# Kernel optimization log

Measured on AMD Instinct MI355X. Metric: run time of the kernel, lower is better.

The kernel has to match this reference:

```python
import jax, jax.numpy as jnp
import numpy as np

B, N, I, K = 2, 8192, 3, 10
LEN_IN = 3 * (K + 1) + 3 * K + I  # 69


def setup_inputs() -> dict:
    key = jax.random.key(0)
    ks = jax.random.split(key, 9)
    return {
        "position": jax.random.normal(ks[0], (B, N, 3), dtype=jnp.float32),
        "velocity": jax.random.normal(ks[1], (B, N, 3), dtype=jnp.float32),
        "init_config": jax.random.normal(ks[2], (B, I), dtype=jnp.float32),
        "W1": jax.random.normal(ks[3], (LEN_IN, 32), dtype=jnp.float32) * 0.1,
        "b1": jnp.zeros((32,), dtype=jnp.float32),
        "W2": jax.random.normal(ks[4], (32, 16), dtype=jnp.float32) * 0.1,
        "b2": jnp.zeros((16,), dtype=jnp.float32),
        "W3": jax.random.normal(ks[5], (16, 6), dtype=jnp.float32) * 0.1,
        "b3": jnp.zeros((6,), dtype=jnp.float32),
    }


def reference(position, velocity, init_config, W1, b1, W2, b2, W3, b3):
    b, n, _ = position.shape
    k = K
    # Squared Euclidean distances (same k-NN ordering as torch.cdist).
    sq = jnp.sum(position * position, axis=-1)  # [B,N]
    d2 = sq[:, :, None] + sq[:, None, :] - 2.0 * jnp.einsum(
        "bnd,bmd->bnm", position, position
    )  # [B,N,N]
    # k+1 nearest (self included), sorted ascending by distance.
    _, idx = jax.lax.top_k(-d2, k + 1)  # [B,N,k+1]
    # Gather neighbor velocities (incl. self) and positions (excl. self).
    vel_nn = jnp.take_along_axis(
        velocity[:, None, :, :], idx[..., None], axis=2
    )  # [B,N,k+1,3]
    pos_nn = jnp.take_along_axis(
        position[:, None, :, :], idx[:, :, 1:, None], axis=2
    )  # [B,N,k,3]
    offset = pos_nn - position[:, :, None, :]  # [B,N,k,3]
    feats = jnp.concatenate(
        [
            vel_nn.reshape(b, n, 3 * (k + 1)),
            offset.reshape(b, n, 3 * k),
            jnp.broadcast_to(init_config[:, None, :], (b, n, init_config.shape[-1])),
        ],
        axis=-1,
    )  # [B,N,6k+3+I]
    h = feats @ W1 + b1
    h = h @ W2 + b2
    pred = h @ W3 + b3  # [B,N,6]
    pred = jnp.concatenate([pred[..., :3] + position, pred[..., 3:]], axis=-1)
    return pred
```

## Files before the change

### kernel.cpp

```cpp
#include <hip/hip_runtime.h>

#define NPTS   8192
#define KNN    11
#define QPB    64
#define NTHR   1024
#define NSLICE 16
#define SLEN   (NPTS / NSLICE)
#define DEPTH  10
#define TRIG   7

__global__ __launch_bounds__(NTHR, 4) void knn_mlp(
    const float* __restrict__ pos,
    const float* __restrict__ vel,
    const float* __restrict__ initc,
    const float* __restrict__ W1,
    const float* __restrict__ b1,
    const float* __restrict__ W2,
    const float* __restrict__ b2,
    const float* __restrict__ W3,
    const float* __restrict__ b3,
    float* __restrict__ out) {

    __shared__ __align__(16) char smem[32 * 1024 + NTHR * DEPTH * 8];
    __shared__ float sW[405];

    float* ssq = (float*)smem;
    unsigned long long* region = (unsigned long long*)(smem + 32 * 1024);

    const int tid  = threadIdx.x;
    const int lane = tid & 63;
    const int wave = tid >> 6;
    const int b    = blockIdx.x >> 7;
    const int n0   = (blockIdx.x & 127) * QPB;
    const int q    = n0 + lane;

    const float* posb = pos + b * NPTS * 3;
    const float* velb = vel + b * NPTS * 3;

    for (int a = tid; a < NPTS; a += NTHR) {
        float x = posb[a * 3 + 0];
        float y = posb[a * 3 + 1];
        float z = posb[a * 3 + 2];
        ssq[a] = __fmaf_rn(z, z, __fmaf_rn(y, y, __fmul_rn(x, x)));
    }
    float* sW12 = (float*)region;
    for (int e = tid; e < 66 * 16; e += NTHR) {
        int r = e >> 4, c = e & 15;
        float s = 0.f;
        for (int j = 0; j < 32; ++j) s += W1[r * 32 + j] * W2[j * 16 + c];
        sW12[e] = s;
    }
    if (tid < 16) {
        float s = b2[tid];
        for (int j = 0; j < 32; ++j) s += b1[j] * W2[j * 16 + tid];
        sW12[66 * 16 + tid] = s;
    }
    if (tid < 3) sW[402 + tid] = initc[b * 3 + tid];
    __syncthreads();
    for (int e = tid; e < 66 * 6; e += NTHR) {
        int r = e / 6, c = e - r * 6;
        float s = 0.f;
        for (int j = 0; j < 16; ++j) s += sW12[r * 16 + j] * W3[j * 6 + c];
        sW[e] = s;
    }
    if (tid < 6) {
        float s = b3[tid];
        for (int j = 0; j < 16; ++j) s += sW12[66 * 16 + j] * W3[j * 6 + tid];
        sW[396 + tid] = s;
    }
    __syncthreads();

    const float qx = posb[q * 3 + 0];
    const float qy = posb[q * 3 + 1];
    const float qz = posb[q * 3 + 2];
    const float sqq = ssq[q];

    float d0 = 3.0e38f, d1 = 3.0e38f, d2v = 3.0e38f, d3 = 3.0e38f, d4 = 3.0e38f,
          d5 = 3.0e38f, d6 = 3.0e38f, d7 = 3.0e38f, d8 = 3.0e38f, d9 = 3.0e38f,
          d10 = 3.0e38f;
    int   i0 = 0x7FFFFFFF, i1 = 0x7FFFFFFF, i2v = 0x7FFFFFFF, i3 = 0x7FFFFFFF,
          i4 = 0x7FFFFFFF, i5 = 0x7FFFFFFF, i6 = 0x7FFFFFFF, i7 = 0x7FFFFFFF,
          i8 = 0x7FFFFFFF, i9 = 0x7FFFFFFF, i10 = 0x7FFFFFFF;

    float thr = 3.0e38f;
    int cnt = 0;

    auto insert = [&](float nd, int nj) {
        if (nd < d10) {
            bool c, cp;
            cp = nd < d9;  d10 = cp ? d9  : nd;             i10 = cp ? i9  : nj;             c = cp;
            cp = nd < d8;  d9  = cp ? d8  : (c ? nd : d9);  i9  = cp ? i8  : (c ? nj : i9);  c = cp;
            cp = nd < d7;  d8  = cp ? d7  : (c ? nd : d8);  i8  = cp ? i7  : (c ? nj : i8);  c = cp;
            cp = nd < d6;  d7  = cp ? d6  : (c ? nd : d7);  i7  = cp ? i6  : (c ? nj : i7);  c = cp;
            cp = nd < d5;  d6  = cp ? d5  : (c ? nd : d6);  i6  = cp ? i5  : (c ? nj : i6);  c = cp;
            cp = nd < d4;  d5  = cp ? d4  : (c ? nd : d5);  i5  = cp ? i4  : (c ? nj : i5);  c = cp;
            cp = nd < d3;  d4  = cp ? d3  : (c ? nd : d4);  i4  = cp ? i3  : (c ? nj : i4);  c = cp;
            cp = nd < d2v; d3  = cp ? d2v : (c ? nd : d3);  i3  = cp ? i2v : (c ? nj : i3);  c = cp;
            cp = nd < d1;  d2v = cp ? d1  : (c ? nd : d2v); i2v = cp ? i1  : (c ? nj : i2v); c = cp;
            cp = nd < d0;  d1  = cp ? d0  : (c ? nd : d1);  i1  = cp ? i0  : (c ? nj : i1);  c = cp;
            if (c) { d0 = nd; i0 = nj; }
        }
    };

    auto flush = [&]() {
#pragma unroll 1
        for (int k = 0; __any(k < cnt); ++k) {
            if (k < cnt) {
                unsigned long long e = region[k * NTHR + tid];
                float nd = __uint_as_float((unsigned)(e >> 32));
                int   nj = (int)(unsigned)(e & 0xFFFFFFFFull);
                insert(nd, nj);
            }
        }
        cnt = 0;
        thr = d10;
    };

    auto proc = [&](float cx, float cy, float cz, float sqc, int j) {
        float dot = __fmaf_rn(qz, cz, __fmaf_rn(qy, cy, __fmul_rn(qx, cx)));
        float dd  = __fmaf_rn(-2.0f, dot, __fadd_rn(sqq, sqc));
        if (dd < thr) {
            region[cnt * NTHR + tid] =
                (((unsigned long long)__float_as_uint(dd)) << 32) | (unsigned)j;
            ++cnt;
        }
    };

    const int base = wave * SLEN;
    const float4* gp = (const float4*)(posb + base * 3);
    const float4* sp = (const float4*)(ssq + base);
#pragma unroll 1
    for (int m = 0; m < SLEN; m += 4) {
        int f = (m >> 2) * 3;
        float4 A = gp[f], Bv = gp[f + 1], C = gp[f + 2];
        float4 S = sp[m >> 2];
        int j = base + m;
        proc(A.x,  A.y,  A.z,  S.x, j + 0);
        proc(A.w,  Bv.x, Bv.y, S.y, j + 1);
        proc(Bv.z, Bv.w, C.x,  S.z, j + 2);
        proc(C.y,  C.z,  C.w,  S.w, j + 3);
        if (__any(cnt >= TRIG)) flush();
    }
    flush();

    __syncthreads();
    float* pd = (float*)smem;
    int*   pi = (int*)(smem + NTHR * KNN * 4);
    {
        float* pw = pd + tid * KNN;
        int*   iw = pi + tid * KNN;
        pw[0] = d0;  pw[1] = d1;  pw[2] = d2v; pw[3] = d3;  pw[4] = d4;
        pw[5] = d5;  pw[6] = d6;  pw[7] = d7;  pw[8] = d8;  pw[9] = d9;
        pw[10] = d10;
        iw[0] = i0;  iw[1] = i1;  iw[2] = i2v; iw[3] = i3;  iw[4] = i4;
        iw[5] = i5;  iw[6] = i6;  iw[7] = i7;  iw[8] = i8;  iw[9] = i9;
        iw[10] = i10;
    }
    __syncthreads();

    if (tid < QPB) {
        int p[NSLICE]; float hd[NSLICE]; int hi[NSLICE];
#pragma unroll
        for (int s = 0; s < NSLICE; ++s) {
            p[s]  = 0;
            hd[s] = pd[(s * 64 + tid) * KNN];
            hi[s] = pi[(s * 64 + tid) * KNN];
        }
        float acc[6];
#pragma unroll
        for (int c = 0; c < 6; ++c) acc[c] = sW[396 + c];

        for (int r = 0; r < KNN; ++r) {
            float bd = 3.9e38f; int bi = 0x7FFFFFFF; int bs = 0;
#pragma unroll
            for (int s = 0; s < NSLICE; ++s) {
                bool better = (hd[s] < bd) || (hd[s] == bd && hi[s] < bi);
                bs = better ? s : bs;
                bi = better ? hi[s] : bi;
                bd = better ? hd[s] : bd;
            }
            {
                int pp = ++p[bs];
                if (pp < KNN) {
                    hd[bs] = pd[(bs * 64 + tid) * KNN + pp];
                    hi[bs] = pi[(bs * 64 + tid) * KNN + pp];
                } else { hd[bs] = 3.9e38f; hi[bs] = 0x7FFFFFFF; }
            }

            int bg = ((unsigned)bi < (unsigned)NPTS) ? bi : 0;

            const float* vp = velb + bg * 3;
            float vx = vp[0], vy = vp[1], vz = vp[2];
            const float* w = &sW[r * 18];
#pragma unroll
            for (int c = 0; c < 6; ++c) {
                acc[c] += vx * w[c];
                acc[c] += vy * w[6 + c];
                acc[c] += vz * w[12 + c];
            }
            if (r >= 1) {
                float ox = posb[bg * 3 + 0] - qx;
                float oy = posb[bg * 3 + 1] - qy;
                float oz = posb[bg * 3 + 2] - qz;
                const float* w2 = &sW[(33 + (r - 1) * 3) * 6];
#pragma unroll
                for (int c = 0; c < 6; ++c) {
                    acc[c] += ox * w2[c];
                    acc[c] += oy * w2[6 + c];
                    acc[c] += oz * w2[12 + c];
                }
            }
        }
#pragma unroll
        for (int k3 = 0; k3 < 3; ++k3) {
            const float* w3 = &sW[(63 + k3) * 6];
            float iv = sW[402 + k3];
#pragma unroll
            for (int c = 0; c < 6; ++c) acc[c] += iv * w3[c];
        }
        acc[0] += qx; acc[1] += qy; acc[2] += qz;

        float* op = out + (b * NPTS + q) * 6;
#pragma unroll
        for (int c = 0; c < 6; ++c) op[c] = acc[c];
    }
}

extern "C" void kernel_launch(void* const* d_in, const int* in_sizes, int n_in,
                              void* d_out, int out_size, void* d_ws, size_t ws_size,
                              hipStream_t stream) {
    (void)in_sizes; (void)n_in; (void)out_size; (void)d_ws; (void)ws_size;
    const float* pos   = (const float*)d_in[0];
    const float* vel   = (const float*)d_in[1];
    const float* initc = (const float*)d_in[2];
    const float* W1    = (const float*)d_in[3];
    const float* b1    = (const float*)d_in[4];
    const float* W2    = (const float*)d_in[5];
    const float* b2    = (const float*)d_in[6];
    const float* W3    = (const float*)d_in[7];
    const float* b3    = (const float*)d_in[8];
    float* out = (float*)d_out;

    knn_mlp<<<256, NTHR, 0, stream>>>(pos, vel, initc, W1, b1, W2, b2, W3, b3, out);
}
```

Baseline: 175.3 us.

## Share per-query kNN thresholds across slice waves at two rendezvous points

Each of the 16 waves scans its own slice of candidates with a private top-11 threshold. The scan is now split into three phases, with two block-wide rendezvous points in between. At each point the waves publish their current 11th-best distance to shared memory, take the minimum across slices, and nudge it up by one ulp so that exact ties are still admitted. That tighter global bound reduces candidate pushes and flushes in later phases, at the cost of two extra __syncthreads and a small shared array.

```diff
diff --git a/kernel.cpp b/kernel.cpp
--- a/kernel.cpp
+++ b/kernel.cpp
@@ -8,6 +8,8 @@
 #define SLEN   (NPTS / NSLICE)
 #define DEPTH  10
 #define TRIG   7
+#define REND1  32
+#define REND2  128
 
 __global__ __launch_bounds__(NTHR, 4) void knn_mlp(
     const float* __restrict__ pos,
@@ -23,6 +25,7 @@
 
     __shared__ __align__(16) char smem[32 * 1024 + NTHR * DEPTH * 8];
     __shared__ float sW[405];
+    __shared__ float thrS[NSLICE][QPB];
 
     float* ssq = (float*)smem;
     unsigned long long* region = (unsigned long long*)(smem + 32 * 1024);
@@ -82,7 +85,8 @@
           i4 = 0x7FFFFFFF, i5 = 0x7FFFFFFF, i6 = 0x7FFFFFFF, i7 = 0x7FFFFFFF,
           i8 = 0x7FFFFFFF, i9 = 0x7FFFFFFF, i10 = 0x7FFFFFFF;
 
-    float thr = 3.0e38f;
+    float thrR = 3.0e38f;
+    float thr  = 3.0e38f;
     int cnt = 0;
 
     auto insert = [&](float nd, int nj) {
@@ -113,7 +117,24 @@
             }
         }
         cnt = 0;
-        thr = d10;
+        thr = fminf(d10, thrR);
+    };
+
+    auto rendezvous = [&]() {
+        flush();
+        thrS[wave][lane] = d10;
+        __syncthreads();
+        float bm = thrS[0][lane];
+#pragma unroll
+        for (int w = 1; w < NSLICE; ++w) bm = fminf(bm, thrS[w][lane]);
+        __syncthreads();
+        unsigned sb = __float_as_uint(bm);
+        unsigned eb = (sb & 0x80000000u) ? ~sb : (sb | 0x80000000u);
+        eb += 1u;
+        float up = (eb & 0x80000000u) ? __uint_as_float(eb & 0x7FFFFFFFu)
+                                      : __uint_as_float(~eb);
+        thrR = fminf(thrR, up);
+        thr  = fminf(d10, thrR);
     };
 
     auto proc = [&](float cx, float cy, float cz, float sqc, int j) {
@@ -130,7 +151,33 @@
     const float4* gp = (const float4*)(posb + base * 3);
     const float4* sp = (const float4*)(ssq + base);
 #pragma unroll 1
-    for (int m = 0; m < SLEN; m += 4) {
+    for (int m = 0; m < REND1; m += 4) {
+        int f = (m >> 2) * 3;
+        float4 A = gp[f], Bv = gp[f + 1], C = gp[f + 2];
+        float4 S = sp[m >> 2];
+        int j = base + m;
+        proc(A.x,  A.y,  A.z,  S.x, j + 0);
+        proc(A.w,  Bv.x, Bv.y, S.y, j + 1);
+        proc(Bv.z, Bv.w, C.x,  S.z, j + 2);
+        proc(C.y,  C.z,  C.w,  S.w, j + 3);
+        if (__any(cnt >= TRIG)) flush();
+    }
+    rendezvous();
+#pragma unroll 1
+    for (int m = REND1; m < REND2; m += 4) {
+        int f = (m >> 2) * 3;
+        float4 A = gp[f], Bv = gp[f + 1], C = gp[f + 2];
+        float4 S = sp[m >> 2];
+        int j = base + m;
+        proc(A.x,  A.y,  A.z,  S.x, j + 0);
+        proc(A.w,  Bv.x, Bv.y, S.y, j + 1);
+        proc(Bv.z, Bv.w, C.x,  S.z, j + 2);
+        proc(C.y,  C.z,  C.w,  S.w, j + 3);
+        if (__any(cnt >= TRIG)) flush();
+    }
+    rendezvous();
+#pragma unroll 1
+    for (int m = REND2; m < SLEN; m += 4) {
         int f = (m >> 2) * 3;
         float4 A = gp[f], Bv = gp[f + 1], C = gp[f + 2];
         float4 S = sp[m >> 2];
```

Result: slower. 211.1 us (+20.4%).
